# Performance work log

Measured on AMD Instinct MI355X. Metric: run time of the kernel, lower is better.

The kernel has to match this reference:

```python
import jax, jax.numpy as jnp
import numpy as np

D_MODEL = 1024
D_FF = 4096
LN_EPS = 1e-5


def _layer_norm(x, gamma, beta):
    mu = jnp.mean(x, axis=-1, keepdims=True)
    var = jnp.mean(jnp.square(x - mu), axis=-1, keepdims=True)
    return (x - mu) * jax.lax.rsqrt(var + LN_EPS) * gamma + beta


def setup_inputs() -> dict:
    key = jax.random.key(0)
    ks = jax.random.split(key, 16)
    B, S, D, F = 2, 2048, D_MODEL, D_FF
    s_d = 1.0 / np.sqrt(D)
    s_f = 1.0 / np.sqrt(F)
    u = lambda k, shape, s: jax.random.uniform(k, shape, jnp.float32, -s, s)
    return {
        "x": jax.random.normal(ks[0], (B, S, D), jnp.float32),
        "wq": u(ks[1], (D, D), s_d), "bq": u(ks[2], (D,), s_d),
        "wk": u(ks[3], (D, D), s_d), "bk": u(ks[4], (D,), s_d),
        "wv": u(ks[5], (D, D), s_d), "bv": u(ks[6], (D,), s_d),
        "wo": u(ks[7], (D, D), s_d), "bo": u(ks[8], (D,), s_d),
        "w1": u(ks[9], (F, D), s_d), "b1": u(ks[10], (F,), s_d),
        "w2": u(ks[11], (D, F), s_f), "b2": u(ks[12], (D,), s_f),
        "g1": jnp.ones((D,), jnp.float32), "be1": jnp.zeros((D,), jnp.float32),
        "g2": jnp.ones((D,), jnp.float32), "be2": jnp.zeros((D,), jnp.float32),
        "num_heads": 16,
    }


def reference(x, wq, bq, wk, bk, wv, bv, wo, bo, w1, b1, w2, b2, g1, be1, g2, be2, num_heads):
    B, S, D = x.shape
    H = num_heads
    dk = D // H
    scale = 1.0 / np.sqrt(dk)

    # --- self-attention (pre-norm) ---
    h = _layer_norm(x, g1, be1)
    q = (h @ wq.T + bq).reshape(B, S, H, dk)
    k = (h @ wk.T + bk).reshape(B, S, H, dk)
    v = (h @ wv.T + bv).reshape(B, S, H, dk)
    scores = jnp.einsum("bqhd,bkhd->bhqk", q, k) * scale  # [B,H,S,S]
    attn = jax.nn.softmax(scores, axis=-1)
    ctx = jnp.einsum("bhqk,bkhd->bqhd", attn, v).reshape(B, S, D)
    x = x + ctx @ wo.T + bo

    # --- feed-forward (pre-norm, exact GELU as in torch default) ---
    h = _layer_norm(x, g2, be2)
    h = jax.nn.gelu(h @ w1.T + b1, approximate=False)
    x = x + h @ w2.T + b2
    return x
```

## Files before the change

kernel.cpp:

```cpp
#include <hip/hip_runtime.h>

typedef __attribute__((ext_vector_type(8))) __bf16 bf16x8;
typedef __attribute__((ext_vector_type(4))) __bf16 bf16x4;
typedef __attribute__((ext_vector_type(4))) float floatx4;
typedef void __attribute__((address_space(3))) lds_void_t;
typedef const void __attribute__((address_space(1))) gbl_void_t;

#define D_MODEL 1024
#define SEQ     2048
#define BATCH   2
#define NH      16
#define DK      64
#define DFF     4096
#define NTOK    (BATCH * SEQ)
#define QKVS    3072

#if __has_builtin(__builtin_amdgcn_exp2f)
#define EXP2(x) __builtin_amdgcn_exp2f(x)
#else
#define EXP2(x) exp2f(x)
#endif

__device__ __forceinline__ float gelu_exact(float x) {
    return 0.5f * x * (1.0f + erff(x * 0.70710678118654752f));
}

__global__ __launch_bounds__(256) void cast_f32_bf16(const float* __restrict__ src,
                                                     __bf16* __restrict__ dst, int n) {
    int i = (blockIdx.x * 256 + threadIdx.x) * 8;
    if (i >= n) return;
    floatx4 a = *(const floatx4*)(src + i);
    floatx4 b = *(const floatx4*)(src + i + 4);
    bf16x8 o;
    for (int j = 0; j < 4; ++j) { o[j] = (__bf16)a[j]; o[4 + j] = (__bf16)b[j]; }
    *(bf16x8*)(dst + i) = o;
}

__global__ __launch_bounds__(64) void ln_kernel(const float* __restrict__ x,
                                                const float* __restrict__ g,
                                                const float* __restrict__ b,
                                                __bf16* __restrict__ out) {
    int row = blockIdx.x, lane = threadIdx.x, base = lane * 16;
    const float* xr = x + (size_t)row * D_MODEL + base;
    float v[16];
    for (int j = 0; j < 4; ++j) {
        floatx4 a = *(const floatx4*)(xr + 4 * j);
        for (int i = 0; i < 4; ++i) v[4 * j + i] = a[i];
    }
    float s = 0.f, sq = 0.f;
    for (int i = 0; i < 16; ++i) { s += v[i]; sq += v[i] * v[i]; }
    for (int o = 1; o < 64; o <<= 1) { s += __shfl_xor(s, o); sq += __shfl_xor(sq, o); }
    float mu = s * (1.0f / D_MODEL);
    float var = sq * (1.0f / D_MODEL) - mu * mu;
    float rstd = rsqrtf(fmaxf(var, 0.f) + 1e-5f);

    const floatx4* gp = (const floatx4*)(g + base);
    const floatx4* bp = (const floatx4*)(b + base);
    bf16x8 o0, o1;
    for (int j = 0; j < 2; ++j) {
        floatx4 gv0 = gp[2 * j], gv1 = gp[2 * j + 1];
        floatx4 bv0 = bp[2 * j], bv1 = bp[2 * j + 1];
        for (int i = 0; i < 4; ++i) {
            float r0 = (v[8 * j + i] - mu) * rstd * gv0[i] + bv0[i];
            float r1 = (v[8 * j + 4 + i] - mu) * rstd * gv1[i] + bv1[i];
            if (j == 0) { o0[i] = (__bf16)r0; o0[4 + i] = (__bf16)r1; }
            else        { o1[i] = (__bf16)r0; o1[4 + i] = (__bf16)r1; }
        }
    }
    bf16x8* op = (bf16x8*)(out + (size_t)row * D_MODEL + base);
    op[0] = o0; op[1] = o1;
}

template <typename OutT, bool GELU, bool TRIBIAS, int KSPLIT>
__global__ __launch_bounds__(256) void gemm_bt(const __bf16* __restrict__ A,
                                               const __bf16* __restrict__ W,
                                               const float* __restrict__ bias0,
                                               const float* __restrict__ bias1,
                                               const float* __restrict__ bias2,
                                               const float* __restrict__ res,
                                               OutT* out, float* part1,
                                               int M, int N, int K) {
    __shared__ __bf16 AsF[2][4096];
    __shared__ __bf16 WsF[2][4096];

    int nwg = gridDim.x * gridDim.y;
    int id = blockIdx.y * gridDim.x + blockIdx.x;
    int cpx = nwg >> 3;
    int swz = (id & 7) * cpx + (id >> 3);
    int m0 = (swz / gridDim.x) * 128, n0 = (swz % gridDim.x) * 128;

    int t = threadIdx.x;
    int lane = t & 63, wave = t >> 6;
    int wm = (wave >> 1) * 64, wn = (wave & 1) * 64;
    int fr = lane & 15, quad = lane >> 4;
    int scol = quad * 8;

    int Ks = K / KSPLIT;
    int kbeg = (KSPLIT > 1) ? blockIdx.z * Ks : 0;

    floatx4 acc[4][4] = {};

    const __bf16* Abase = A + kbeg;
    const __bf16* Wbase = W + kbeg;

    auto stage = [&](int buf, int k0) {
#pragma unroll
        for (int p = 0; p < 2; ++p) {
            int blk = p * 4 + wave;
            int row = (blk >> 2) * 64 + (blk & 3) * 16 + fr;
            __builtin_amdgcn_global_load_lds(
                (gbl_void_t*)(Abase + (size_t)(m0 + row) * K + k0 + scol),
                (lds_void_t*)&AsF[buf][blk * 512], 16, 0, 0);
            __builtin_amdgcn_global_load_lds(
                (gbl_void_t*)(Wbase + (size_t)(n0 + row) * K + k0 + scol),
                (lds_void_t*)&WsF[buf][blk * 512], 16, 0, 0);
        }
    };

    auto compute = [&](int buf) {
        bf16x8 af[4], wf[4];
#pragma unroll
        for (int i = 0; i < 4; ++i)
            af[i] = *(const bf16x8*)&AsF[buf][((wave >> 1) * 4 + i) * 512 + lane * 8];
#pragma unroll
        for (int i = 0; i < 4; ++i)
            wf[i] = *(const bf16x8*)&WsF[buf][((wave & 1) * 4 + i) * 512 + lane * 8];
#pragma unroll
        for (int mi = 0; mi < 4; ++mi)
#pragma unroll
            for (int ni = 0; ni < 4; ++ni)
                acc[mi][ni] = __builtin_amdgcn_mfma_f32_16x16x32_bf16(af[mi], wf[ni], acc[mi][ni], 0, 0, 0);
    };

    int nsteps = Ks / 32;
    stage(0, 0);
    for (int s = 0; s < nsteps; ++s) {
        int cur = s & 1;
        __syncthreads();
        if (s + 1 < nsteps) stage(cur ^ 1, (s + 1) * 32);
        compute(cur);
    }

    if (KSPLIT > 1) {
        float* pb = (blockIdx.z == 0) ? (float*)out : part1;
#pragma unroll
        for (int ni = 0; ni < 4; ++ni) {
            int col = n0 + wn + ni * 16 + fr;
#pragma unroll
            for (int mi = 0; mi < 4; ++mi)
#pragma unroll
                for (int r = 0; r < 4; ++r) {
                    int row = m0 + wm + mi * 16 + quad * 4 + r;
                    pb[(size_t)row * N + col] = acc[mi][ni][r];
                }
        }
    } else {
#pragma unroll
        for (int ni = 0; ni < 4; ++ni) {
            int col = n0 + wn + ni * 16 + fr;
            const float* bp = bias0;
            int bcol = col;
            if (TRIBIAS) { bp = col < 1024 ? bias0 : (col < 2048 ? bias1 : bias2); bcol = col & 1023; }
            float bv = bp[bcol];
#pragma unroll
            for (int mi = 0; mi < 4; ++mi) {
#pragma unroll
                for (int r = 0; r < 4; ++r) {
                    int row = m0 + wm + mi * 16 + quad * 4 + r;
                    float v = acc[mi][ni][r] + bv;
                    if (GELU) v = gelu_exact(v);
                    if (res) v += res[(size_t)row * N + col];
                    out[(size_t)row * N + col] = (OutT)v;
                }
            }
        }
    }
}

__global__ __launch_bounds__(256) void reduce_k2(const float* __restrict__ p0,
                                                 const float* p1,
                                                 const float* __restrict__ res,
                                                 const float* __restrict__ bias,
                                                 float* out) {
    int i = (blockIdx.x * 256 + threadIdx.x) * 4;
    floatx4 a = *(const floatx4*)(p0 + i);
    floatx4 b = *(const floatx4*)(p1 + i);
    floatx4 r = *(const floatx4*)(res + i);
    floatx4 bv = *(const floatx4*)(bias + (i & 1023));
    floatx4 o;
#pragma unroll
    for (int j = 0; j < 4; ++j) o[j] = a[j] + b[j] + r[j] + bv[j];
    *(floatx4*)(out + i) = o;
}

__global__ __launch_bounds__(256) void transpose_v(const __bf16* __restrict__ qkv,
                                                   __bf16* __restrict__ vt) {
    __shared__ __bf16 tile[64][72];
    int b = blockIdx.z, h = blockIdx.y, s0 = blockIdx.x * 64;
    int t = threadIdx.x;
    int dl = (t & 7) * 8, sl = t >> 3;
    for (int p = 0; p < 2; ++p) {
        int s = sl + p * 32;
        bf16x8 val = *(const bf16x8*)(qkv + (size_t)(b * SEQ + s0 + s) * QKVS + 2048 + h * DK + dl);
        *(bf16x8*)&tile[s][dl] = val;
    }
    __syncthreads();
    int sl2 = (t & 7) * 8, d = t >> 3;
    for (int p = 0; p < 2; ++p) {
        int dd = d + p * 32;
        bf16x8 val;
        for (int j = 0; j < 8; ++j) val[j] = tile[sl2 + j][dd];
        *(bf16x8*)(vt + ((size_t)(b * NH + h) * DK + dd) * SEQ + s0 + sl2) = val;
    }
}

__global__ __launch_bounds__(256, 2) void attn_kernel(const __bf16* __restrict__ qkv,
                                                      const __bf16* __restrict__ vt,
                                                      __bf16* __restrict__ ctx) {
    __shared__ __bf16 Klds[8192];
    __shared__ __bf16 Vlds[8192];
    __shared__ __bf16 Plds[4][32][136];
    int b = blockIdx.z, h = blockIdx.y;
    int wave = threadIdx.x >> 6, lane = threadIdx.x & 63;
    int q0 = blockIdx.x * 128 + wave * 32;
    int fr = lane & 15, quad = lane >> 4;
    const float sc2 = 0.18033688011112042f;

    const __bf16* qp0 = qkv + (size_t)(b * SEQ + q0 + fr) * QKVS + h * DK + quad * 8;
    const __bf16* qp1 = qp0 + (size_t)16 * QKVS;
    bf16x8 qA0 = *(const bf16x8*)qp0, qB0 = *(const bf16x8*)(qp0 + 32);
    bf16x8 qA1 = *(const bf16x8*)qp1, qB1 = *(const bf16x8*)(qp1 + 32);

    const __bf16* kg = qkv + (size_t)b * SEQ * QKVS + 1024 + h * DK;
    const __bf16* vg = vt + (size_t)(b * NH + h) * DK * SEQ;

    floatx4 o[8] = {};
    float m0q = -1e30f, l0q = 0.f, m1q = -1e30f, l1q = 0.f;

    auto stage_tile = [&](int k0) {
#pragma unroll
        for (int p = 0; p < 4; ++p) {
            int bid = wave * 4 + p;
            int f = bid >> 1, half = bid & 1;
            __builtin_amdgcn_global_load_lds(
                (gbl_void_t*)(kg + (size_t)(k0 + f * 16 + fr) * QKVS + quad * 8 + half * 32),
                (lds_void_t*)&Klds[bid * 512], 16, 0, 0);
            int c = bid >> 2, ti = bid & 3;
            __builtin_amdgcn_global_load_lds(
                (gbl_void_t*)(vg + (size_t)(ti * 16 + fr) * SEQ + k0 + c * 32 + quad * 8),
                (lds_void_t*)&Vlds[bid * 512], 16, 0, 0);
        }
    };

    stage_tile(0);
    __syncthreads();

    for (int k0 = 0; k0 < SEQ; k0 += 128) {
        const __bf16* Kb = Klds + lane * 8;
        const __bf16* Vb = Vlds + lane * 8;
        bf16x8 kA[8], kB[8];
#pragma unroll
        for (int f = 0; f < 8; ++f) {
            kA[f] = *(const bf16x8*)(Kb + (f * 2 + 0) * 512);
            kB[f] = *(const bf16x8*)(Kb + (f * 2 + 1) * 512);
        }

        floatx4 s[8];
#pragma unroll
        for (int f = 0; f < 8; ++f) {
            floatx4 z = {0.f, 0.f, 0.f, 0.f};
            z = __builtin_amdgcn_mfma_f32_16x16x32_bf16(kA[f], qA0, z, 0, 0, 0);
            s[f] = __builtin_amdgcn_mfma_f32_16x16x32_bf16(kB[f], qB0, z, 0, 0, 0);
        }
        {
            float fm[8];
#pragma unroll
            for (int f = 0; f < 8; ++f)
                fm[f] = fmaxf(fmaxf(s[f][0], s[f][1]), fmaxf(s[f][2], s[f][3]));
            float mx = fmaxf(fmaxf(fmaxf(fm[0], fm[1]), fmaxf(fm[2], fm[3])),
                             fmaxf(fmaxf(fm[4], fm[5]), fmaxf(fm[6], fm[7])));
            float mx2 = mx * sc2;
            mx2 = fmaxf(mx2, __shfl_xor(mx2, 16));
            mx2 = fmaxf(mx2, __shfl_xor(mx2, 32));
            float mn = fmaxf(m0q, mx2);
            float alpha = EXP2(m0q - mn);
            m0q = mn;
            float r0 = 0.f, r1 = 0.f, r2 = 0.f, r3 = 0.f;
#pragma unroll
            for (int f = 0; f < 8; ++f) {
                bf16x4 pk;
                float p0 = EXP2(fmaf(s[f][0], sc2, -mn));
                float p1 = EXP2(fmaf(s[f][1], sc2, -mn));
                float p2 = EXP2(fmaf(s[f][2], sc2, -mn));
                float p3 = EXP2(fmaf(s[f][3], sc2, -mn));
                r0 += p0; r1 += p1; r2 += p2; r3 += p3;
                pk[0] = (__bf16)p0; pk[1] = (__bf16)p1; pk[2] = (__bf16)p2; pk[3] = (__bf16)p3;
                *(bf16x4*)&Plds[wave][fr][f * 16 + quad * 4] = pk;
            }
            float rs = (r0 + r1) + (r2 + r3);
            rs += __shfl_xor(rs, 16);
            rs += __shfl_xor(rs, 32);
            l0q = l0q * alpha + rs;
            float aB[4];
#pragma unroll
            for (int r = 0; r < 4; ++r) aB[r] = __shfl(alpha, quad * 4 + r);
#pragma unroll
            for (int ti = 0; ti < 4; ++ti)
#pragma unroll
                for (int r = 0; r < 4; ++r) o[ti][r] *= aB[r];
        }

        floatx4 s1[8];
#pragma unroll
        for (int f = 0; f < 8; ++f) {
            floatx4 z = {0.f, 0.f, 0.f, 0.f};
            z = __builtin_amdgcn_mfma_f32_16x16x32_bf16(kA[f], qA1, z, 0, 0, 0);
            s1[f] = __builtin_amdgcn_mfma_f32_16x16x32_bf16(kB[f], qB1, z, 0, 0, 0);
        }

        bf16x8 vf[4][4];
#pragma unroll
        for (int c = 0; c < 4; ++c)
#pragma unroll
            for (int ti = 0; ti < 4; ++ti)
                vf[c][ti] = *(const bf16x8*)(Vb + (c * 4 + ti) * 512);

        __syncthreads();
        if (k0 + 128 < SEQ) stage_tile(k0 + 128);

        {
            float fm[8];
#pragma unroll
            for (int f = 0; f < 8; ++f)
                fm[f] = fmaxf(fmaxf(s1[f][0], s1[f][1]), fmaxf(s1[f][2], s1[f][3]));
            float mx = fmaxf(fmaxf(fmaxf(fm[0], fm[1]), fmaxf(fm[2], fm[3])),
                             fmaxf(fmaxf(fm[4], fm[5]), fmaxf(fm[6], fm[7])));
            float mx2 = mx * sc2;
            mx2 = fmaxf(mx2, __shfl_xor(mx2, 16));
            mx2 = fmaxf(mx2, __shfl_xor(mx2, 32));
            float mn = fmaxf(m1q, mx2);
            float alpha = EXP2(m1q - mn);
            m1q = mn;
            float r0 = 0.f, r1 = 0.f, r2 = 0.f, r3 = 0.f;
#pragma unroll
            for (int f = 0; f < 8; ++f) {
                bf16x4 pk;
                float p0 = EXP2(fmaf(s1[f][0], sc2, -mn));
                float p1 = EXP2(fmaf(s1[f][1], sc2, -mn));
                float p2 = EXP2(fmaf(s1[f][2], sc2, -mn));
                float p3 = EXP2(fmaf(s1[f][3], sc2, -mn));
                r0 += p0; r1 += p1; r2 += p2; r3 += p3;
                pk[0] = (__bf16)p0; pk[1] = (__bf16)p1; pk[2] = (__bf16)p2; pk[3] = (__bf16)p3;
                *(bf16x4*)&Plds[wave][16 + fr][f * 16 + quad * 4] = pk;
            }
            float rs = (r0 + r1) + (r2 + r3);
            rs += __shfl_xor(rs, 16);
            rs += __shfl_xor(rs, 32);
            l1q = l1q * alpha + rs;
            float aB[4];
#pragma unroll
            for (int r = 0; r < 4; ++r) aB[r] = __shfl(alpha, quad * 4 + r);
#pragma unroll
            for (int ti = 0; ti < 4; ++ti)
#pragma unroll
                for (int r = 0; r < 4; ++r) o[4 + ti][r] *= aB[r];
        }
        __threadfence_block();

        bf16x8 pa0[4], pa1[4];
#pragma unroll
        for (int c = 0; c < 4; ++c) {
            pa0[c] = *(const bf16x8*)&Plds[wave][fr][c * 32 + quad * 8];
            pa1[c] = *(const bf16x8*)&Plds[wave][16 + fr][c * 32 + quad * 8];
        }
#pragma unroll
        for (int c = 0; c < 4; ++c)
#pragma unroll
            for (int ti = 0; ti < 4; ++ti) {
                o[ti]     = __builtin_amdgcn_mfma_f32_16x16x32_bf16(pa0[c], vf[c][ti], o[ti], 0, 0, 0);
                o[4 + ti] = __builtin_amdgcn_mfma_f32_16x16x32_bf16(pa1[c], vf[c][ti], o[4 + ti], 0, 0, 0);
            }
        __threadfence_block();

        __syncthreads();
    }
    float lB0[4], lB1[4];
#pragma unroll
    for (int r = 0; r < 4; ++r) {
        lB0[r] = __shfl(l0q, quad * 4 + r);
        lB1[r] = __shfl(l1q, quad * 4 + r);
    }
#pragma unroll
    for (int ti = 0; ti < 4; ++ti)
#pragma unroll
        for (int r = 0; r < 4; ++r) {
            ctx[(size_t)(b * SEQ + q0 + quad * 4 + r) * D_MODEL + h * DK + ti * 16 + fr] =
                (__bf16)(o[ti][r] / lB0[r]);
            ctx[(size_t)(b * SEQ + q0 + 16 + quad * 4 + r) * D_MODEL + h * DK + ti * 16 + fr] =
                (__bf16)(o[4 + ti][r] / lB1[r]);
        }
}

extern "C" void kernel_launch(void* const* d_in, const int* in_sizes, int n_in,
                              void* d_out, int out_size, void* d_ws, size_t ws_size,
                              hipStream_t stream) {
    const float* x   = (const float*)d_in[0];
    const float* wq  = (const float*)d_in[1];
    const float* bq  = (const float*)d_in[2];
    const float* wk  = (const float*)d_in[3];
    const float* bk  = (const float*)d_in[4];
    const float* wv  = (const float*)d_in[5];
    const float* bv  = (const float*)d_in[6];
    const float* wo  = (const float*)d_in[7];
    const float* bo  = (const float*)d_in[8];
    const float* w1  = (const float*)d_in[9];
    const float* b1  = (const float*)d_in[10];
    const float* w2  = (const float*)d_in[11];
    const float* b2  = (const float*)d_in[12];
    const float* g1  = (const float*)d_in[13];
    const float* be1 = (const float*)d_in[14];
    const float* g2  = (const float*)d_in[15];
    const float* be2 = (const float*)d_in[16];
    float* out = (float*)d_out;

    char* ws = (char*)d_ws;
    const size_t MB = 1024 * 1024;
    __bf16* wqkvB = (__bf16*)(ws);
    __bf16* woB   = (__bf16*)(ws + 6 * MB);
    __bf16* w1B   = (__bf16*)(ws + 8 * MB);
    __bf16* w2B   = (__bf16*)(ws + 16 * MB);
    __bf16* h1    = (__bf16*)(ws + 24 * MB);
    float*  x1    = (float*)(ws + 24 * MB);
    __bf16* qkv   = (__bf16*)(ws + 40 * MB);
    __bf16* vt    = (__bf16*)(ws + 64 * MB);
    __bf16* ffh   = (__bf16*)(ws + 40 * MB);
    float*  pA0   = (float*)(ws + 40 * MB);
    float*  pA1   = (float*)(ws + 56 * MB);
    float*  pF0   = (float*)(ws);
    __bf16* ctx   = (__bf16*)d_out;
    __bf16* h2    = (__bf16*)d_out;

    const int NDD = D_MODEL * D_MODEL;
    const int NDF = D_MODEL * DFF;
    cast_f32_bf16<<<NDD / 2048, 256, 0, stream>>>(wq, wqkvB, NDD);
    cast_f32_bf16<<<NDD / 2048, 256, 0, stream>>>(wk, wqkvB + NDD, NDD);
    cast_f32_bf16<<<NDD / 2048, 256, 0, stream>>>(wv, wqkvB + 2 * NDD, NDD);
    cast_f32_bf16<<<NDD / 2048, 256, 0, stream>>>(wo, woB, NDD);
    cast_f32_bf16<<<NDF / 2048, 256, 0, stream>>>(w1, w1B, NDF);
    cast_f32_bf16<<<NDF / 2048, 256, 0, stream>>>(w2, w2B, NDF);

    dim3 gQKV(QKVS / 128, NTOK / 128);
    dim3 gDz(D_MODEL / 128, NTOK / 128, 2);
    dim3 gF(DFF / 128, NTOK / 128);
    dim3 gTr(SEQ / 64, NH, BATCH);
    dim3 gAttn(SEQ / 128, NH, BATCH);
    int gRed = NTOK * D_MODEL / (256 * 4);

    ln_kernel<<<NTOK, 64, 0, stream>>>(x, g1, be1, h1);
    gemm_bt<__bf16, false, true, 1><<<gQKV, 256, 0, stream>>>(h1, wqkvB, bq, bk, bv, nullptr, qkv, nullptr, NTOK, QKVS, D_MODEL);
    transpose_v<<<gTr, 256, 0, stream>>>(qkv, vt);
    attn_kernel<<<gAttn, 256, 0, stream>>>(qkv, vt, ctx);
    gemm_bt<float, false, false, 2><<<gDz, 256, 0, stream>>>(ctx, woB, nullptr, nullptr, nullptr, nullptr, pA0, pA1, NTOK, D_MODEL, D_MODEL);
    reduce_k2<<<gRed, 256, 0, stream>>>(pA0, pA1, x, bo, x1);
    ln_kernel<<<NTOK, 64, 0, stream>>>(x1, g2, be2, h2);
    gemm_bt<__bf16, true, false, 1><<<gF, 256, 0, stream>>>(h2, w1B, b1, b1, b1, nullptr, ffh, nullptr, NTOK, DFF, D_MODEL);
    gemm_bt<float, false, false, 2><<<gDz, 256, 0, stream>>>(ffh, w2B, nullptr, nullptr, nullptr, nullptr, pF0, (float*)d_out, NTOK, D_MODEL, DFF);
    reduce_k2<<<gRed, 256, 0, stream>>>(pF0, (float*)d_out, x1, b2, out);
}
```

Measured before the change: 471.8 us.

## Merge weight casts into one launch, fuse reduce with LayerNorm, drop tile swizzle

The six per-weight cast launches become a single cast_all kernel that picks source and destination by block index. The split-K reduction after the output projection is fused with the second LayerNorm into one row kernel, which removes one launch and a full read of x1. The GEMM also drops its XCD-aware block swizzle and maps tiles directly from blockIdx, which may hurt L2 locality across chiplets.

```diff
diff --git a/kernel.cpp b/kernel.cpp
--- a/kernel.cpp
+++ b/kernel.cpp
@@ -25,10 +25,28 @@
     return 0.5f * x * (1.0f + erff(x * 0.70710678118654752f));
 }
 
-__global__ __launch_bounds__(256) void cast_f32_bf16(const float* __restrict__ src,
-                                                     __bf16* __restrict__ dst, int n) {
-    int i = (blockIdx.x * 256 + threadIdx.x) * 8;
-    if (i >= n) return;
+__global__ __launch_bounds__(256) void cast_all(const float* __restrict__ wq,
+                                                const float* __restrict__ wk,
+                                                const float* __restrict__ wv,
+                                                const float* __restrict__ wo,
+                                                const float* __restrict__ w1,
+                                                const float* __restrict__ w2,
+                                                __bf16* __restrict__ wqkvB,
+                                                __bf16* __restrict__ woB,
+                                                __bf16* __restrict__ w1B,
+                                                __bf16* __restrict__ w2B) {
+    int blk = blockIdx.x;
+    const float* src;
+    __bf16* dst;
+    int base;
+    const int NDD8 = (D_MODEL * D_MODEL) / 2048;
+    if (blk < NDD8)          { src = wq; dst = wqkvB;                     base = blk; }
+    else if (blk < 2 * NDD8) { src = wk; dst = wqkvB + D_MODEL * D_MODEL; base = blk - NDD8; }
+    else if (blk < 3 * NDD8) { src = wv; dst = wqkvB + 2 * D_MODEL * D_MODEL; base = blk - 2 * NDD8; }
+    else if (blk < 4 * NDD8) { src = wo; dst = woB;                       base = blk - 3 * NDD8; }
+    else if (blk < 8 * NDD8) { src = w1; dst = w1B;                       base = blk - 4 * NDD8; }
+    else                     { src = w2; dst = w2B;                       base = blk - 8 * NDD8; }
+    int i = (base * 256 + threadIdx.x) * 8;
     floatx4 a = *(const floatx4*)(src + i);
     floatx4 b = *(const floatx4*)(src + i + 4);
     bf16x8 o;
@@ -71,6 +89,50 @@
     op[0] = o0; op[1] = o1;
 }
 
+__global__ __launch_bounds__(64) void reduce_ln(const float* __restrict__ p0,
+                                                const float* __restrict__ p1,
+                                                const float* __restrict__ res,
+                                                const float* __restrict__ bias,
+                                                const float* __restrict__ g,
+                                                const float* __restrict__ be,
+                                                float* __restrict__ x1,
+                                                __bf16* __restrict__ h2) {
+    int row = blockIdx.x, lane = threadIdx.x, base = lane * 16;
+    size_t off = (size_t)row * D_MODEL + base;
+    float v[16];
+    for (int j = 0; j < 4; ++j) {
+        floatx4 a = *(const floatx4*)(p0 + off + 4 * j);
+        floatx4 b = *(const floatx4*)(p1 + off + 4 * j);
+        floatx4 r = *(const floatx4*)(res + off + 4 * j);
+        floatx4 bv = *(const floatx4*)(bias + base + 4 * j);
+        floatx4 o;
+        for (int i = 0; i < 4; ++i) { o[i] = a[i] + b[i] + r[i] + bv[i]; v[4 * j + i] = o[i]; }
+        *(floatx4*)(x1 + off + 4 * j) = o;
+    }
+    float s = 0.f, sq = 0.f;
+    for (int i = 0; i < 16; ++i) { s += v[i]; sq += v[i] * v[i]; }
+    for (int o = 1; o < 64; o <<= 1) { s += __shfl_xor(s, o); sq += __shfl_xor(sq, o); }
+    float mu = s * (1.0f / D_MODEL);
+    float var = sq * (1.0f / D_MODEL) - mu * mu;
+    float rstd = rsqrtf(fmaxf(var, 0.f) + 1e-5f);
+
+    const floatx4* gp = (const floatx4*)(g + base);
+    const floatx4* bp = (const floatx4*)(be + base);
+    bf16x8 o0, o1;
+    for (int j = 0; j < 2; ++j) {
+        floatx4 gv0 = gp[2 * j], gv1 = gp[2 * j + 1];
+        floatx4 bv0 = bp[2 * j], bv1 = bp[2 * j + 1];
+        for (int i = 0; i < 4; ++i) {
+            float r0 = (v[8 * j + i] - mu) * rstd * gv0[i] + bv0[i];
+            float r1 = (v[8 * j + 4 + i] - mu) * rstd * gv1[i] + bv1[i];
+            if (j == 0) { o0[i] = (__bf16)r0; o0[4 + i] = (__bf16)r1; }
+            else        { o1[i] = (__bf16)r0; o1[4 + i] = (__bf16)r1; }
+        }
+    }
+    bf16x8* op = (bf16x8*)(h2 + off);
+    op[0] = o0; op[1] = o1;
+}
+
 template <typename OutT, bool GELU, bool TRIBIAS, int KSPLIT>
 __global__ __launch_bounds__(256) void gemm_bt(const __bf16* __restrict__ A,
                                                const __bf16* __restrict__ W,
@@ -83,12 +145,7 @@
     __shared__ __bf16 AsF[2][4096];
     __shared__ __bf16 WsF[2][4096];
 
-    int nwg = gridDim.x * gridDim.y;
-    int id = blockIdx.y * gridDim.x + blockIdx.x;
-    int cpx = nwg >> 3;
-    int swz = (id & 7) * cpx + (id >> 3);
-    int m0 = (swz / gridDim.x) * 128, n0 = (swz % gridDim.x) * 128;
-
+    int m0 = blockIdx.y * 128, n0 = blockIdx.x * 128;
     int t = threadIdx.x;
     int lane = t & 63, wave = t >> 6;
     int wm = (wave >> 1) * 64, wn = (wave & 1) * 64;
@@ -440,15 +497,6 @@
     __bf16* ctx   = (__bf16*)d_out;
     __bf16* h2    = (__bf16*)d_out;
 
-    const int NDD = D_MODEL * D_MODEL;
-    const int NDF = D_MODEL * DFF;
-    cast_f32_bf16<<<NDD / 2048, 256, 0, stream>>>(wq, wqkvB, NDD);
-    cast_f32_bf16<<<NDD / 2048, 256, 0, stream>>>(wk, wqkvB + NDD, NDD);
-    cast_f32_bf16<<<NDD / 2048, 256, 0, stream>>>(wv, wqkvB + 2 * NDD, NDD);
-    cast_f32_bf16<<<NDD / 2048, 256, 0, stream>>>(wo, woB, NDD);
-    cast_f32_bf16<<<NDF / 2048, 256, 0, stream>>>(w1, w1B, NDF);
-    cast_f32_bf16<<<NDF / 2048, 256, 0, stream>>>(w2, w2B, NDF);
-
     dim3 gQKV(QKVS / 128, NTOK / 128);
     dim3 gDz(D_MODEL / 128, NTOK / 128, 2);
     dim3 gF(DFF / 128, NTOK / 128);
@@ -456,13 +504,13 @@
     dim3 gAttn(SEQ / 128, NH, BATCH);
     int gRed = NTOK * D_MODEL / (256 * 4);
 
+    cast_all<<<6144, 256, 0, stream>>>(wq, wk, wv, wo, w1, w2, wqkvB, woB, w1B, w2B);
     ln_kernel<<<NTOK, 64, 0, stream>>>(x, g1, be1, h1);
     gemm_bt<__bf16, false, true, 1><<<gQKV, 256, 0, stream>>>(h1, wqkvB, bq, bk, bv, nullptr, qkv, nullptr, NTOK, QKVS, D_MODEL);
     transpose_v<<<gTr, 256, 0, stream>>>(qkv, vt);
     attn_kernel<<<gAttn, 256, 0, stream>>>(qkv, vt, ctx);
     gemm_bt<float, false, false, 2><<<gDz, 256, 0, stream>>>(ctx, woB, nullptr, nullptr, nullptr, nullptr, pA0, pA1, NTOK, D_MODEL, D_MODEL);
-    reduce_k2<<<gRed, 256, 0, stream>>>(pA0, pA1, x, bo, x1);
-    ln_kernel<<<NTOK, 64, 0, stream>>>(x1, g2, be2, h2);
+    reduce_ln<<<NTOK, 64, 0, stream>>>(pA0, pA1, x, bo, g2, be2, x1, h2);
     gemm_bt<__bf16, true, false, 1><<<gF, 256, 0, stream>>>(h2, w1B, b1, b1, b1, nullptr, ffh, nullptr, NTOK, DFF, D_MODEL);
     gemm_bt<float, false, false, 2><<<gDz, 256, 0, stream>>>(ffh, w2B, nullptr, nullptr, nullptr, nullptr, pF0, (float*)d_out, NTOK, D_MODEL, DFF);
     reduce_k2<<<gRed, 256, 0, stream>>>(pF0, (float*)d_out, x1, b2, out);
```

Result: faster. 462.2 us (-2.0%).
